# Optimization experiments

Hardware: AMD Instinct MI355X
Metric: run time of the kernel (lower is better)

Reference implementation:

```python
import jax, jax.numpy as jnp
import numpy as np

N_NODES = 10000
N_EDGES = 160000
MUL = 32                 # multiplicity, equal across irreps (asserted in torch code)
IR_DIMS = [1, 3, 5]      # 2l+1 for l=0,1,2
N_DIM = MUL * sum(IR_DIMS)   # 288
NODE_ATTR_DIM = 64
HEAD_DIM = 32
N_SCALARS = MUL * 1      # irreps_mul * n_l[0] = 32
ISQRTD = 5               # math.isqrt(32) == 5 (integer sqrt, as in original)
HIDDEN = [64, 64]


def _mlp_params(key, dims):
    ps = []
    for i in range(len(dims) - 1):
        key, k1, k2 = jax.random.split(key, 3)
        W = jax.random.normal(k1, (dims[i], dims[i + 1]), jnp.float32) / np.sqrt(dims[i])
        b = jnp.zeros((dims[i + 1],), jnp.float32)
        ps += [W, b]
    return ps


def setup_inputs() -> dict:
    key = jax.random.key(0)
    k1, k2, k3, k4, k5 = jax.random.split(key, 5)
    edge_feat = jax.random.normal(k1, (N_EDGES, N_DIM), jnp.float32)
    node_attrs = jax.random.normal(k2, (N_NODES, NODE_ATTR_DIM), jnp.float32)
    edge_center = jax.random.randint(k3, (N_EDGES,), 0, N_NODES, jnp.int32)
    qp = _mlp_params(k4, [NODE_ATTR_DIM] + HIDDEN + [N_SCALARS * HEAD_DIM])
    kp = _mlp_params(k5, [N_SCALARS] + HIDDEN + [N_SCALARS * HEAD_DIM])
    return {
        "edge_feat": edge_feat, "node_attrs": node_attrs, "edge_center": edge_center,
        "Wq0": qp[0], "bq0": qp[1], "Wq1": qp[2], "bq1": qp[3], "Wq2": qp[4], "bq2": qp[5],
        "Wk0": kp[0], "bk0": kp[1], "Wk1": kp[2], "bk1": kp[3], "Wk2": kp[4], "bk2": kp[5],
    }


def _mlp(x, W0, b0, W1, b1, W2, b2):
    x = jax.nn.silu(x @ W0 + b0)
    x = jax.nn.silu(x @ W1 + b1)
    return x @ W2 + b2


def _reshape_irreps(x):  # [E, 288] -> [E, MUL, 9]
    parts, off = [], 0
    for d in IR_DIMS:
        parts.append(x[:, off:off + MUL * d].reshape(-1, MUL, d))
        off += MUL * d
    return jnp.concatenate(parts, axis=-1)


def _inverse_reshape_irreps(x):  # [E, MUL, 9] -> [E, 288]
    parts, off = [], 0
    for d in IR_DIMS:
        parts.append(x[:, :, off:off + d].reshape(-1, MUL * d))
        off += d
    return jnp.concatenate(parts, axis=-1)


def _segment_softmax(w, seg, num_segments):  # w: [E, C]
    m = jax.ops.segment_max(w, seg, num_segments=num_segments)
    e = jnp.exp(w - m[seg])
    z = jax.ops.segment_sum(e, seg, num_segments=num_segments)
    return e / z[seg]


def reference(edge_feat, node_attrs, edge_center,
              Wq0, bq0, Wq1, bq1, Wq2, bq2,
              Wk0, bk0, Wk1, bk1, Wk2, bk2):
    # gather node attrs per edge, compute Q
    Q = _mlp(node_attrs[edge_center], Wq0, bq0, Wq1, bq1, Wq2, bq2)
    Q = Q.reshape(-1, N_SCALARS, HEAD_DIM)
    # K from scalar channels of edge features
    K = _mlp(edge_feat[:, :N_SCALARS], Wk0, bk0, Wk1, bk1, Wk2, bk2)
    K = K.reshape(-1, N_SCALARS, HEAD_DIM)
    # attention logits, scaled by integer sqrt of head_dim (as in original)
    W = jnp.einsum('ecd,ecd->ec', Q, K) * ISQRTD
    attn = _segment_softmax(W, edge_center, N_NODES)       # [E, MUL]
    ef = _reshape_irreps(edge_feat)                        # [E, MUL, 9]
    ef = ef * attn[:, :, None]
    ef = _inverse_reshape_irreps(ef)                       # [E, 288]
    out = jax.ops.segment_sum(ef, edge_center, num_segments=N_NODES)
    return out
```

## Files before the change

kernel.cpp:

```cpp
#include <hip/hip_runtime.h>
#include <hip/hip_bf16.h>
#include <math.h>

#define NN 10000
#define NE 160000
#define ND 288


__device__ __forceinline__ float silu_f(float x){ return x / (1.0f + __expf(-x)); }

__global__ void k_hist(const int* __restrict__ ec, int* __restrict__ cnt){
    int e = blockIdx.x*256 + threadIdx.x;
    if (e < NE) atomicAdd(&cnt[ec[e]], 1);
}

__global__ void k_scan(const int* __restrict__ cnt, int* __restrict__ offs){
    __shared__ int part[1024];
    int tid = threadIdx.x;
    int base = tid*10;
    int s = 0;
    #pragma unroll
    for (int i=0;i<10;i++){ int idx=base+i; s += (idx<NN)? cnt[idx] : 0; }
    part[tid] = s;
    __syncthreads();
    for (int off=1; off<1024; off<<=1){
        int v = (tid>=off)? part[tid-off] : 0;
        __syncthreads();
        part[tid] += v;
        __syncthreads();
    }
    int run = part[tid] - s;
    for (int i=0;i<10;i++){ int idx=base+i; if(idx<NN){ offs[idx]=run; run += cnt[idx]; } }
    if (tid==1023) offs[NN] = part[1023];
}

__global__ void k_scatter(const int* __restrict__ ec, const int* __restrict__ offs,
                          int* __restrict__ cur, int* __restrict__ sorted){
    int e = blockIdx.x*256 + threadIdx.x;
    if (e < NE){
        int n = ec[e];
        int p = offs[n] + atomicAdd(&cur[n], 1);
        sorted[p] = e;
    }
}

__global__ void k_T(const float* __restrict__ Wq2, const float* __restrict__ Wk2,
                    float* __restrict__ T){
    int idx = blockIdx.x*256 + threadIdx.x;
    int c = idx & 31, j = (idx>>5) & 63, i = idx >> 11;
    const float* a = Wq2 + i*1024 + c*32;
    const float* b = Wk2 + j*1024 + c*32;
    float s = 0.f;
    #pragma unroll
    for (int d=0; d<32; d++) s += a[d]*b[d];
    T[idx] = 5.0f*s;
}

__global__ void k_U(const float* __restrict__ bq2, const float* __restrict__ Wk2,
                    float* __restrict__ U){
    int idx = blockIdx.x*256 + threadIdx.x;
    int j = idx>>5, c = idx&31; float s=0.f;
    #pragma unroll
    for (int d=0; d<32; d++) s += bq2[c*32+d]*Wk2[j*1024 + c*32 + d];
    U[idx] = 5.0f*s;
}

__global__ __launch_bounds__(256) void k_H(const float* __restrict__ na,
                    const float* __restrict__ Wq0, const float* __restrict__ bq0,
                    const float* __restrict__ Wq1, const float* __restrict__ bq1,
                    float* __restrict__ Hq){
    __shared__ float W0s[4096], W1s[4096];
    __shared__ float as[4][64], h1s[4][64];
    int tid = threadIdx.x;
    for (int i=tid; i<4096; i+=256){ W0s[i]=Wq0[i]; W1s[i]=Wq1[i]; }
    int sg = tid>>6, lane = tid&63;
    int n = blockIdx.x*4 + sg;
    if (n < NN) as[sg][lane] = na[(size_t)n*64 + lane];
    __syncthreads();
    if (n < NN){
        float s = bq0[lane];
        #pragma unroll
        for (int i=0;i<64;i++) s += as[sg][i]*W0s[i*64+lane];
        h1s[sg][lane] = silu_f(s);
    }
    __syncthreads();
    if (n < NN){
        float s = bq1[lane];
        #pragma unroll
        for (int i=0;i<64;i++) s += h1s[sg][i]*W1s[i*64+lane];
        Hq[(size_t)n*64 + lane] = silu_f(s);
    }
}

__global__ __launch_bounds__(256) void k_kmlp(
        const float* __restrict__ ef, const int* __restrict__ sorted,
        const float* __restrict__ Wk0, const float* __restrict__ bk0,
        const float* __restrict__ Wk1, const float* __restrict__ bk1,
        float* __restrict__ h2g){
    __shared__ float xs[64*33];
    __shared__ float h1s[64*65];
    __shared__ float h2s[64*66];
    __shared__ int   es[64];
    int tid = threadIdx.x;
    int p0 = blockIdx.x*64;
    if (tid < 64) es[tid] = sorted[p0+tid];
    __syncthreads();
    for (int idx=tid; idx<2048; idx+=256){
        int k = idx>>5, i = idx&31;
        xs[k*33+i] = ef[(size_t)es[k]*ND + i];
    }
    __syncthreads();
    int e = tid & 63;
    int o0 = __builtin_amdgcn_readfirstlane((tid>>6)*16);
    {
        float acc[16];
        #pragma unroll
        for (int t=0;t<16;t++) acc[t] = bk0[o0+t];
        for (int i=0;i<32;i++){
            float xv = xs[e*33+i];
            const float* wr = Wk0 + i*64 + o0;
            #pragma unroll
            for (int t=0;t<16;t++) acc[t] = fmaf(xv, wr[t], acc[t]);
        }
        #pragma unroll
        for (int t=0;t<16;t++) h1s[e*65+o0+t] = silu_f(acc[t]);
    }
    __syncthreads();
    {
        float acc[16];
        #pragma unroll
        for (int t=0;t<16;t++) acc[t] = bk1[o0+t];
        for (int j=0;j<64;j++){
            float hv = h1s[e*65+j];
            const float* wr = Wk1 + j*64 + o0;
            #pragma unroll
            for (int t=0;t<16;t++) acc[t] = fmaf(hv, wr[t], acc[t]);
        }
        #pragma unroll
        for (int t=0;t<16;t++) h2s[e*66+o0+t] = silu_f(acc[t]);
    }
    __syncthreads();
    for (int idx=tid; idx<4096; idx+=256)
        h2g[(size_t)p0*64 + idx] = h2s[(idx>>6)*66 + (idx&63)];
}

__global__ __launch_bounds__(256) void k_M(
        const float* __restrict__ Hq, const float* __restrict__ T,
        const float* __restrict__ U, float* __restrict__ M){
    __shared__ float hs[64*65];
    int tid = threadIdx.x;
    int n0 = blockIdx.x*64;
    int jc = blockIdx.y*256 + (tid&63)*4;
    for (int idx=tid; idx<4096; idx+=256){
        int nn = idx>>6, i = idx&63;
        int n = n0+nn;
        hs[nn*65+i] = Hq[(size_t)(n<NN?n:NN-1)*64 + i];
    }
    __syncthreads();
    int tg = __builtin_amdgcn_readfirstlane(tid>>6)*16;
    float4 uv = *(const float4*)&U[jc];
    float acc[16][4];
    #pragma unroll
    for (int t=0;t<16;t++){ acc[t][0]=uv.x; acc[t][1]=uv.y; acc[t][2]=uv.z; acc[t][3]=uv.w; }
    for (int i=0;i<64;i++){
        float4 tv = *(const float4*)&T[i*2048 + jc];
        #pragma unroll
        for (int t=0;t<16;t++){
            float hv = hs[(tg+t)*65 + i];
            acc[t][0] = fmaf(hv, tv.x, acc[t][0]);
            acc[t][1] = fmaf(hv, tv.y, acc[t][1]);
            acc[t][2] = fmaf(hv, tv.z, acc[t][2]);
            acc[t][3] = fmaf(hv, tv.w, acc[t][3]);
        }
    }
    #pragma unroll
    for (int t=0;t<16;t++){
        int n = n0 + tg + t;
        if (n < NN){
            float4 o; o.x=acc[t][0]; o.y=acc[t][1]; o.z=acc[t][2]; o.w=acc[t][3];
            *(float4*)&M[(size_t)n*2048 + jc] = o;
        }
    }
}

__global__ __launch_bounds__(256) void k_logit(
        const float* __restrict__ h2g, const float* __restrict__ Mg,
        const int* __restrict__ sorted, const int* __restrict__ ec,
        float* __restrict__ Lg){
    __shared__ float h2s[64*65];
    __shared__ int ns[64];
    int tid = threadIdx.x;
    int p0 = blockIdx.x*64;
    if (tid < 64) ns[tid] = ec[sorted[p0+tid]];
    for (int idx=tid; idx<4096; idx+=256)
        h2s[(idx>>6)*65 + (idx&63)] = h2g[(size_t)p0*64 + idx];
    __syncthreads();
    int e = tid>>2, cq = (tid&3)*8;
    const float* Mn = Mg + (size_t)ns[e]*2048 + cq;
    float acc[8];
    #pragma unroll
    for (int t=0;t<8;t++) acc[t]=0.f;
    for (int j=0;j<64;j++){
        float hv = h2s[e*65+j];
        float4 m0 = *(const float4*)&Mn[j*32];
        float4 m1 = *(const float4*)&Mn[j*32+4];
        acc[0] = fmaf(hv, m0.x, acc[0]);
        acc[1] = fmaf(hv, m0.y, acc[1]);
        acc[2] = fmaf(hv, m0.z, acc[2]);
        acc[3] = fmaf(hv, m0.w, acc[3]);
        acc[4] = fmaf(hv, m1.x, acc[4]);
        acc[5] = fmaf(hv, m1.y, acc[5]);
        acc[6] = fmaf(hv, m1.z, acc[6]);
        acc[7] = fmaf(hv, m1.w, acc[7]);
    }
    float* lp = Lg + (size_t)(p0+e)*32 + cq;
    float4 o0; o0.x=acc[0]; o0.y=acc[1]; o0.z=acc[2]; o0.w=acc[3];
    float4 o1; o1.x=acc[4]; o1.y=acc[5]; o1.z=acc[6]; o1.w=acc[7];
    *(float4*)lp = o0;
    *(float4*)(lp+4) = o1;
}

__global__ __launch_bounds__(320) void k_node(
        const float* __restrict__ ef, const float* __restrict__ Lg,
        const int* __restrict__ offs, const int* __restrict__ sorted,
        float* __restrict__ out){
    __shared__ float Ls[64*32];
    __shared__ float msh[32], zsh[32], rsh[32];
    __shared__ int   es[64];

    int tid = threadIdx.x;
    int n = blockIdx.x;
    int o0 = offs[n], count = offs[n+1] - o0;
    if (tid < 32){ msh[tid] = -INFINITY; zsh[tid] = 0.f; rsh[tid] = 0.f; }
    int col = tid;
    int chcol = (col<32)? col : (col<128)? (col-32)/3 : (col-128)/5;
    float acc0 = 0.f;
    __syncthreads();

    for (int base=0; base<count; base+=64){
        int ne = min(64, count-base);
        if (tid < 64) es[tid] = (tid < ne) ? sorted[o0+base+tid] : 0;
        for (int idx=tid; idx<ne*32; idx+=320)
            Ls[idx] = Lg[(size_t)(o0+base)*32 + idx];
        __syncthreads();
        if (tid < 32){
            int c = tid;
            float mold = msh[c], lmax = mold;
            for (int k=0;k<ne;k++) lmax = fmaxf(lmax, Ls[k*32+c]);
            float rr = __expf(mold - lmax);
            float zz = zsh[c]*rr;
            for (int k=0;k<ne;k++){
                float pp = __expf(Ls[k*32+c] - lmax);
                Ls[k*32+c] = pp; zz += pp;
            }
            zsh[c]=zz; msh[c]=lmax; rsh[c]=rr;
        }
        __syncthreads();
        if (tid < 288){
            acc0 *= rsh[chcol];
            int k = 0;
            for (; k+4<=ne; k+=4){
                int e0=es[k], e1=es[k+1], e2=es[k+2], e3=es[k+3];
                float p0=Ls[k*32+chcol],     p1=Ls[(k+1)*32+chcol];
                float p2=Ls[(k+2)*32+chcol], p3=Ls[(k+3)*32+chcol];
                float v0=ef[(size_t)e0*ND+col], v1=ef[(size_t)e1*ND+col];
                float v2=ef[(size_t)e2*ND+col], v3=ef[(size_t)e3*ND+col];
                acc0 = fmaf(p0,v0,acc0); acc0 = fmaf(p1,v1,acc0);
                acc0 = fmaf(p2,v2,acc0); acc0 = fmaf(p3,v3,acc0);
            }
            for (; k<ne; k++)
                acc0 = fmaf(Ls[k*32+chcol], ef[(size_t)es[k]*ND+col], acc0);
        }
        __syncthreads();
    }
    if (tid < 288)
        out[(size_t)n*ND + col] = (count>0) ? acc0/zsh[chcol] : 0.f;
}

extern "C" void kernel_launch(void* const* d_in, const int* in_sizes, int n_in,
                              void* d_out, int out_size, void* d_ws, size_t ws_size,
                              hipStream_t stream) {
    const float* edge_feat  = (const float*)d_in[0];
    const float* node_attrs = (const float*)d_in[1];
    const int*   edge_center= (const int*)  d_in[2];
    const float* Wq0 = (const float*)d_in[3];  const float* bq0 = (const float*)d_in[4];
    const float* Wq1 = (const float*)d_in[5];  const float* bq1 = (const float*)d_in[6];
    const float* Wq2 = (const float*)d_in[7];  const float* bq2 = (const float*)d_in[8];
    const float* Wk0 = (const float*)d_in[9];  const float* bk0 = (const float*)d_in[10];
    const float* Wk1 = (const float*)d_in[11]; const float* bk1 = (const float*)d_in[12];
    const float* Wk2 = (const float*)d_in[13]; const float* bk2 = (const float*)d_in[14];
    float* out = (float*)d_out;

    float* T    = (float*)d_ws;
    float* U    = T + 131072;
    float* Hq   = U + 2048;
    float* h2g  = Hq + (size_t)NN*64;
    float* M    = h2g + (size_t)NE*64;
    float* Lg   = M + (size_t)NN*2048;
    int*   cnt  = (int*)(Lg + (size_t)NE*32);
    int*   cur  = cnt + NN;
    int*   offs = cur + NN;
    int*   sorted = offs + NN + 1;

    hipMemsetAsync(cnt, 0, 2*NN*sizeof(int), stream);

    k_hist   <<<(NE+255)/256, 256, 0, stream>>>(edge_center, cnt);
    k_scan   <<<1, 1024, 0, stream>>>(cnt, offs);
    k_scatter<<<(NE+255)/256, 256, 0, stream>>>(edge_center, offs, cur, sorted);
    k_T      <<<512, 256, 0, stream>>>(Wq2, Wk2, T);
    k_U      <<<8, 256, 0, stream>>>(bq2, Wk2, U);
    k_H      <<<(NN+3)/4, 256, 0, stream>>>(node_attrs, Wq0, bq0, Wq1, bq1, Hq);
    k_kmlp   <<<NE/64, 256, 0, stream>>>(edge_feat, sorted, Wk0, bk0, Wk1, bk1, h2g);
    k_M      <<<dim3((NN+63)/64, 8), 256, 0, stream>>>(Hq, T, U, M);
    k_logit  <<<NE/64, 256, 0, stream>>>(h2g, M, sorted, edge_center, Lg);
    k_node   <<<NN, 320, 0, stream>>>(edge_feat, Lg, offs, sorted, out);
}
```

Before: 489.8 us.

## Fuse logit computation into per-node softmax-aggregate kernel, merge T/U kernels

Removes the separate k_logit kernel and computes each node's edge logits inside k_node. Each block stages the node's 64x32 M slice and the h2 rows of its edges in shared memory, then runs a small register-tiled matmul on 64 threads. This drops the Lg round-trip and the per-edge re-gather of M rows from global memory. In exchange the edge chunk shrinks from 64 to 32, and only 64 of 320 threads do the logit matmul while the rest sit idle. The change also merges the k_T and k_U kernels into one launch and vectorises the h2 store in k_kmlp.

```diff
diff --git a/kernel.cpp b/kernel.cpp
--- a/kernel.cpp
+++ b/kernel.cpp
@@ -5,6 +5,8 @@
 #define NN 10000
 #define NE 160000
 #define ND 288
+#define EC 32
+#define H2P 36
 
 
 __device__ __forceinline__ float silu_f(float x){ return x / (1.0f + __expf(-x)); }
@@ -44,25 +46,25 @@
     }
 }
 
-__global__ void k_T(const float* __restrict__ Wq2, const float* __restrict__ Wk2,
-                    float* __restrict__ T){
+__global__ void k_TU(const float* __restrict__ Wq2, const float* __restrict__ Wk2,
+                     const float* __restrict__ bq2,
+                     float* __restrict__ T, float* __restrict__ U){
     int idx = blockIdx.x*256 + threadIdx.x;
-    int c = idx & 31, j = (idx>>5) & 63, i = idx >> 11;
-    const float* a = Wq2 + i*1024 + c*32;
-    const float* b = Wk2 + j*1024 + c*32;
-    float s = 0.f;
-    #pragma unroll
-    for (int d=0; d<32; d++) s += a[d]*b[d];
-    T[idx] = 5.0f*s;
-}
-
-__global__ void k_U(const float* __restrict__ bq2, const float* __restrict__ Wk2,
-                    float* __restrict__ U){
-    int idx = blockIdx.x*256 + threadIdx.x;
-    int j = idx>>5, c = idx&31; float s=0.f;
-    #pragma unroll
-    for (int d=0; d<32; d++) s += bq2[c*32+d]*Wk2[j*1024 + c*32 + d];
-    U[idx] = 5.0f*s;
+    if (idx < 131072){
+        int c = idx & 31, j = (idx>>5) & 63, i = idx >> 11;
+        const float* a = Wq2 + i*1024 + c*32;
+        const float* b = Wk2 + j*1024 + c*32;
+        float s = 0.f;
+        #pragma unroll
+        for (int d=0; d<32; d++) s += a[d]*b[d];
+        T[idx] = 5.0f*s;
+    } else if (idx < 133120){
+        int t = idx - 131072;
+        int j = t>>5, c = t&31; float s=0.f;
+        #pragma unroll
+        for (int d=0; d<32; d++) s += bq2[c*32+d]*Wk2[j*1024 + c*32 + d];
+        U[t] = 5.0f*s;
+    }
 }
 
 __global__ __launch_bounds__(256) void k_H(const float* __restrict__ na,
@@ -140,8 +142,13 @@
         for (int t=0;t<16;t++) h2s[e*66+o0+t] = silu_f(acc[t]);
     }
     __syncthreads();
-    for (int idx=tid; idx<4096; idx+=256)
-        h2g[(size_t)p0*64 + idx] = h2s[(idx>>6)*66 + (idx&63)];
+    for (int idx=tid; idx<1024; idx+=256){
+        int k = idx>>4, q = idx&15;
+        float4 v;
+        v.x = h2s[k*66 + q*4+0]; v.y = h2s[k*66 + q*4+1];
+        v.z = h2s[k*66 + q*4+2]; v.w = h2s[k*66 + q*4+3];
+        *(float4*)&h2g[(size_t)(p0+k)*64 + q*4] = v;
+    }
 }
 
 __global__ __launch_bounds__(256) void k_M(
@@ -183,65 +190,66 @@
     }
 }
 
-__global__ __launch_bounds__(256) void k_logit(
-        const float* __restrict__ h2g, const float* __restrict__ Mg,
-        const int* __restrict__ sorted, const int* __restrict__ ec,
-        float* __restrict__ Lg){
-    __shared__ float h2s[64*65];
-    __shared__ int ns[64];
-    int tid = threadIdx.x;
-    int p0 = blockIdx.x*64;
-    if (tid < 64) ns[tid] = ec[sorted[p0+tid]];
-    for (int idx=tid; idx<4096; idx+=256)
-        h2s[(idx>>6)*65 + (idx&63)] = h2g[(size_t)p0*64 + idx];
-    __syncthreads();
-    int e = tid>>2, cq = (tid&3)*8;
-    const float* Mn = Mg + (size_t)ns[e]*2048 + cq;
-    float acc[8];
-    #pragma unroll
-    for (int t=0;t<8;t++) acc[t]=0.f;
-    for (int j=0;j<64;j++){
-        float hv = h2s[e*65+j];
-        float4 m0 = *(const float4*)&Mn[j*32];
-        float4 m1 = *(const float4*)&Mn[j*32+4];
-        acc[0] = fmaf(hv, m0.x, acc[0]);
-        acc[1] = fmaf(hv, m0.y, acc[1]);
-        acc[2] = fmaf(hv, m0.z, acc[2]);
-        acc[3] = fmaf(hv, m0.w, acc[3]);
-        acc[4] = fmaf(hv, m1.x, acc[4]);
-        acc[5] = fmaf(hv, m1.y, acc[5]);
-        acc[6] = fmaf(hv, m1.z, acc[6]);
-        acc[7] = fmaf(hv, m1.w, acc[7]);
-    }
-    float* lp = Lg + (size_t)(p0+e)*32 + cq;
-    float4 o0; o0.x=acc[0]; o0.y=acc[1]; o0.z=acc[2]; o0.w=acc[3];
-    float4 o1; o1.x=acc[4]; o1.y=acc[5]; o1.z=acc[6]; o1.w=acc[7];
-    *(float4*)lp = o0;
-    *(float4*)(lp+4) = o1;
-}
-
 __global__ __launch_bounds__(320) void k_node(
-        const float* __restrict__ ef, const float* __restrict__ Lg,
+        const float* __restrict__ ef, const float* __restrict__ h2g,
+        const float* __restrict__ Mg,
         const int* __restrict__ offs, const int* __restrict__ sorted,
         float* __restrict__ out){
-    __shared__ float Ls[64*32];
+    __shared__ float Ms[2048];
+    __shared__ float h2sT[64*H2P];
+    __shared__ float Ls[EC*32];
     __shared__ float msh[32], zsh[32], rsh[32];
-    __shared__ int   es[64];
+    __shared__ int   es[EC];
 
     int tid = threadIdx.x;
     int n = blockIdx.x;
     int o0 = offs[n], count = offs[n+1] - o0;
+    {
+        const float4* m4 = (const float4*)(Mg + (size_t)n*2048);
+        float4* s4 = (float4*)Ms;
+        for (int idx=tid; idx<512; idx+=320) s4[idx] = m4[idx];
+    }
     if (tid < 32){ msh[tid] = -INFINITY; zsh[tid] = 0.f; rsh[tid] = 0.f; }
     int col = tid;
     int chcol = (col<32)? col : (col<128)? (col-32)/3 : (col-128)/5;
+    if (chcol > 31) chcol = 31;
     float acc0 = 0.f;
     __syncthreads();
 
-    for (int base=0; base<count; base+=64){
-        int ne = min(64, count-base);
-        if (tid < 64) es[tid] = (tid < ne) ? sorted[o0+base+tid] : 0;
-        for (int idx=tid; idx<ne*32; idx+=320)
-            Ls[idx] = Lg[(size_t)(o0+base)*32 + idx];
+    for (int base=0; base<count; base+=EC){
+        int ne = min(EC, count-base);
+        if (tid < EC) es[tid] = (tid < ne) ? sorted[o0+base+tid] : 0;
+        for (int idx=tid; idx<2048; idx+=320){
+            int k = idx>>6, j = idx&63;
+            h2sT[j*H2P + k] = (k < ne) ? h2g[(size_t)(o0+base+k)*64 + j] : 0.f;
+        }
+        __syncthreads();
+        if (tid < 64){
+            int k0 = (tid&7)*4, c0 = (tid>>3)*4;
+            float acc[4][4];
+            #pragma unroll
+            for (int kk=0;kk<4;kk++){
+                #pragma unroll
+                for (int cc=0;cc<4;cc++) acc[kk][cc] = 0.f;
+            }
+            for (int j=0;j<64;j++){
+                float4 va = *(const float4*)&h2sT[j*H2P + k0];
+                float4 vm = *(const float4*)&Ms[j*32 + c0];
+                float vak[4] = {va.x, va.y, va.z, va.w};
+                #pragma unroll
+                for (int kk=0;kk<4;kk++){
+                    acc[kk][0] = fmaf(vak[kk], vm.x, acc[kk][0]);
+                    acc[kk][1] = fmaf(vak[kk], vm.y, acc[kk][1]);
+                    acc[kk][2] = fmaf(vak[kk], vm.z, acc[kk][2]);
+                    acc[kk][3] = fmaf(vak[kk], vm.w, acc[kk][3]);
+                }
+            }
+            #pragma unroll
+            for (int kk=0;kk<4;kk++){
+                float4 o; o.x=acc[kk][0]; o.y=acc[kk][1]; o.z=acc[kk][2]; o.w=acc[kk][3];
+                *(float4*)&Ls[(k0+kk)*32 + c0] = o;
+            }
+        }
         __syncthreads();
         if (tid < 32){
             int c = tid;
@@ -296,8 +304,7 @@
     float* Hq   = U + 2048;
     float* h2g  = Hq + (size_t)NN*64;
     float* M    = h2g + (size_t)NE*64;
-    float* Lg   = M + (size_t)NN*2048;
-    int*   cnt  = (int*)(Lg + (size_t)NE*32);
+    int*   cnt  = (int*)(M + (size_t)NN*2048);
     int*   cur  = cnt + NN;
     int*   offs = cur + NN;
     int*   sorted = offs + NN + 1;
@@ -307,11 +314,9 @@
     k_hist   <<<(NE+255)/256, 256, 0, stream>>>(edge_center, cnt);
     k_scan   <<<1, 1024, 0, stream>>>(cnt, offs);
     k_scatter<<<(NE+255)/256, 256, 0, stream>>>(edge_center, offs, cur, sorted);
-    k_T      <<<512, 256, 0, stream>>>(Wq2, Wk2, T);
-    k_U      <<<8, 256, 0, stream>>>(bq2, Wk2, U);
+    k_TU     <<<520, 256, 0, stream>>>(Wq2, Wk2, bq2, T, U);
     k_H      <<<(NN+3)/4, 256, 0, stream>>>(node_attrs, Wq0, bq0, Wq1, bq1, Hq);
     k_kmlp   <<<NE/64, 256, 0, stream>>>(edge_feat, sorted, Wk0, bk0, Wk1, bk1, h2g);
     k_M      <<<dim3((NN+63)/64, 8), 256, 0, stream>>>(Hq, T, U, M);
-    k_logit  <<<NE/64, 256, 0, stream>>>(h2g, M, sorted, edge_center, Lg);
-    k_node   <<<NN, 320, 0, stream>>>(edge_feat, Lg, offs, sorted, out);
-}
+    k_node   <<<NN, 320, 0, stream>>>(edge_feat, h2g, M, offs, sorted, out);
+}
```

New measurement: 524.7 us. 1.07x slower.
